# Performance work log

Hardware: AMD Instinct MI355X
Metric: run time of the kernel (lower is better)

Reference implementation:

```python
import jax, jax.numpy as jnp
import numpy as np
from jax import lax

P = (8, 10)        # partition size (p0, p1) for all four types
NUM_HEADS = 32
CURV = 1.0
EPS = 1e-5


def _ln(x, w, b):
    m = x.mean(-1, keepdims=True)
    v = ((x - m) ** 2).mean(-1, keepdims=True)
    return (x - m) / jnp.sqrt(v + EPS) * w + b


def _partition(x, p, mode):
    B, c, T, V = x.shape
    p0, p1 = p
    if mode == 1:
        y = x.reshape(B, c, T // p0, p0, V // p1, p1).transpose(0, 2, 4, 3, 5, 1)
    elif mode == 2:
        y = x.reshape(B, c, T // p0, p0, p1, V // p1).transpose(0, 2, 5, 3, 4, 1)
    elif mode == 3:
        y = x.reshape(B, c, p0, T // p0, V // p1, p1).transpose(0, 3, 4, 2, 5, 1)
    else:
        y = x.reshape(B, c, p0, T // p0, p1, V // p1).transpose(0, 3, 5, 2, 4, 1)
    return y.reshape(-1, p0, p1, c)


def _reverse(parts, B, TV, p, mode):
    T, V = TV
    p0, p1 = p
    y = parts.reshape(B, T // p0, V // p1, p0, p1, -1)
    perm = {1: (0, 5, 1, 3, 2, 4), 2: (0, 5, 1, 3, 4, 2),
            3: (0, 5, 3, 1, 2, 4), 4: (0, 5, 3, 1, 4, 2)}[mode]
    return y.transpose(perm).reshape(B, -1, T, V)


def _euc_to_poincare(x):
    n = jnp.maximum(jnp.linalg.norm(x, axis=-1, keepdims=True), 1e-10)
    return (-1.0 / CURV) * jnp.tanh(-CURV * n) * x / n


def _poincare_to_euc(x):
    n = jnp.clip(jnp.linalg.norm(x, axis=-1, keepdims=True), 1e-10, 1 - 1e-5)
    return jnp.arctanh(n * (-1.0 / CURV)) * x / n


def _linear_attention(x, h):
    # x: [Bw, N, 3*h*d]  (fused qkv channels)
    Bw, N, c3 = x.shape
    d = c3 // (3 * h)
    qkv = x.reshape(Bw, N, 3, h, d).transpose(2, 0, 3, 1, 4)  # [3,Bw,h,N,d]
    q = qkv[0] * (h ** -0.5)
    k, v = qkv[1], qkv[2]
    kv = jax.nn.softmax(jnp.einsum('bhnd,bhne->bhde', k, v), axis=-1)  # [Bw,h,d,d]
    attn = jnp.einsum('bhni,bhmi->bhnm', q, kv)                        # q @ kv^T
    return attn.transpose(0, 2, 1, 3).reshape(Bw, N, h * d)


def setup_inputs() -> dict:
    key = jax.random.key(0)
    ks = jax.random.split(key, 8)
    B, C, T, V = 32, 256, 64, 50
    s = 0.02
    return {
        'x': jax.random.normal(ks[0], (B, C, T, V), jnp.float32),
        'norm1_w': jnp.ones((C,), jnp.float32),
        'norm1_b': jnp.zeros((C,), jnp.float32),
        'map_w': jax.random.normal(ks[1], (C, 2 * C), jnp.float32) * s,
        'map_b': jnp.zeros((2 * C,), jnp.float32),
        'gconv': jax.random.normal(ks[2], (NUM_HEADS // 4, V, V), jnp.float32) * s,
        'tconv_w': jax.random.normal(ks[3], (C // 4, (C // 4) // (NUM_HEADS // 4), 7, 1), jnp.float32) * s,
        'tconv_b': jnp.zeros((C // 4,), jnp.float32),
        'proj_w': jax.random.normal(ks[4], (C, C), jnp.float32) * s,
        'proj_b': jnp.zeros((C,), jnp.float32),
        'norm2_w': jnp.ones((C,), jnp.float32),
        'norm2_b': jnp.zeros((C,), jnp.float32),
        'mlp_w1': jax.random.normal(ks[5], (C, 4 * C), jnp.float32) * s,
        'mlp_b1': jnp.zeros((4 * C,), jnp.float32),
        'mlp_w2': jax.random.normal(ks[6], (4 * C, C), jnp.float32) * s,
        'mlp_b2': jnp.zeros((C,), jnp.float32),
    }


def reference(x, norm1_w, norm1_b, map_w, map_b, gconv, tconv_w, tconv_b,
              proj_w, proj_b, norm2_w, norm2_b, mlp_w1, mlp_b1, mlp_w2, mlp_b2):
    B, C, T, V = x.shape
    xi = x.transpose(0, 2, 3, 1)                 # [B,T,V,C]
    skip = xi
    f = (_ln(xi, norm1_w, norm1_b) @ map_w + map_b).transpose(0, 3, 1, 2)  # [B,2C,T,V]
    f_conv, f_attn = f[:, :C // 2], f[:, C // 2:]
    fg, ft = f_conv[:, :C // 4], f_conv[:, C // 4:]
    G = gconv.shape[0]
    # learned graph conv over joints V (grouped over channels)
    y_g = jnp.einsum('bgctu,gvu->bgctv', fg.reshape(B, G, -1, T, V), gconv).reshape(B, -1, T, V)
    # grouped temporal conv (kernel_size x 1)
    y_t = lax.conv_general_dilated(ft, tconv_w, (1, 1), [(3, 3), (0, 0)],
                                   dimension_numbers=('NCHW', 'OIHW', 'NCHW'),
                                   feature_group_count=G) + tconv_b[None, :, None, None]
    ys = [y_g, y_t]
    ca = f_attn.shape[1] // 4                    # 3C/8 per branch (fused qkv)
    h = NUM_HEADS // 8
    for i in range(4):
        fa = f_attn[:, i * ca:(i + 1) * ca]
        parts = _partition(fa, P, i + 1).reshape(-1, P[0] * P[1], ca)
        a = _poincare_to_euc(_linear_attention(_euc_to_poincare(parts), h))
        ys.append(_reverse(a, B, (T, V), P, i + 1))
    out = jnp.concatenate(ys, axis=1).transpose(0, 2, 3, 1) @ proj_w + proj_b
    out = skip + out
    hmid = jax.nn.gelu(_ln(out, norm2_w, norm2_b) @ mlp_w1 + mlp_b1, approximate=False)
    out = out + (hmid @ mlp_w2 + mlp_b2)
    return out.transpose(0, 3, 1, 2)
```

## Files before the change

### kernel.cpp

```cpp
#include <hip/hip_runtime.h>
#include <hip/hip_bf16.h>
#include <math.h>

#define BB  32
#define TVV 3200
#define XB  819200

typedef __attribute__((ext_vector_type(8))) short s8v;
typedef __attribute__((ext_vector_type(4))) float f4v;
typedef unsigned short u16;
typedef unsigned int   u32;

__device__ __forceinline__ u16 f2bf(float f) {
  __hip_bfloat16 h = __float2bfloat16(f);
  union { __hip_bfloat16 h; u16 u; } cv; cv.h = h; return cv.u;
}
__device__ __forceinline__ float bf2f(u16 u) {
  return __uint_as_float(((u32)u) << 16);
}

__device__ __forceinline__ void glds16(const u16* g, u16* l) {
  __builtin_amdgcn_global_load_lds((const __attribute__((address_space(1))) u32*)g,
                                   (__attribute__((address_space(3))) u32*)l, 16, 0, 0);
}

template<int K>
__device__ __forceinline__ void gemm_core(const u16* __restrict__ A, const u16* __restrict__ B,
                                          int m0, int n0, u16* sA, u16* sB, f4v (&acc)[4][4]) {
  const int tid = threadIdx.x, lane = tid & 63, wave = tid >> 6;
  const int wr = wave >> 1, wc = wave & 1;
  const int q = lane >> 4, l15 = lane & 15;
  const int srow = lane >> 2;
  const int skq  = (lane & 3) << 3;
  const u16* gA = A + (size_t)(m0 + wave * 32 + srow) * K + skq;
  const u16* gB = B + (size_t)(n0 + wave * 32 + srow) * K + skq;
  u16* lA = sA + wave * 1024;
  u16* lB = sB + wave * 1024;
  for (int k0 = 0; k0 < K; k0 += 32) {
    glds16(gA + k0,                 lA);
    glds16(gA + k0 + (size_t)16 * K, lA + 512);
    glds16(gB + k0,                 lB);
    glds16(gB + k0 + (size_t)16 * K, lB + 512);
    __syncthreads();
    s8v af[4], bfr[4];
#pragma unroll
    for (int i = 0; i < 4; ++i) {
      af[i]  = *(const s8v*)(sA + (wr * 64 + i * 16 + l15) * 32 + q * 8);
      bfr[i] = *(const s8v*)(sB + (wc * 64 + i * 16 + l15) * 32 + q * 8);
    }
#pragma unroll
    for (int mi = 0; mi < 4; ++mi)
#pragma unroll
      for (int ni = 0; ni < 4; ++ni)
        acc[mi][ni] = __builtin_amdgcn_mfma_f32_16x16x32_bf16(af[mi], bfr[ni], acc[mi][ni], 0, 0, 0);
    __syncthreads();
  }
}

__global__ __launch_bounds__(256)
void k_wprep(const float* __restrict__ src, u16* __restrict__ dst, int K, int N) {
  int idx = blockIdx.x * 256 + threadIdx.x;
  if (idx >= N * K) return;
  int n = idx / K, k = idx - n * K;
  dst[idx] = f2bf(src[(size_t)k * N + n]);
}

__global__ __launch_bounds__(256)
void k_lnx(const float* __restrict__ x, int b0, const float* __restrict__ w,
           const float* __restrict__ bias, float* __restrict__ xtok, u16* __restrict__ xln) {
  __shared__ float sx[32][264];
  __shared__ float srs_[32][33], srq_[32][33];
  __shared__ float smu[32], sst[32];
  int m0 = blockIdx.x * 32;
  int b = b0 + m0 / TVV, tv0 = m0 % TVV;
  int tid = threadIdx.x;
  int qd = tid & 7, c = tid >> 3;
  const float* xb = x + (size_t)b * XB + tv0;
  float wreg = w[tid], breg = bias[tid];
  float s[4] = {0.f, 0.f, 0.f, 0.f}, ss[4] = {0.f, 0.f, 0.f, 0.f};
#pragma unroll
  for (int k = 0; k < 8; ++k) {
    int cc = k * 32 + c;
    float4 vv = *(const float4*)(xb + (size_t)cc * TVV + qd * 4);
    sx[qd * 4 + 0][cc] = vv.x; sx[qd * 4 + 1][cc] = vv.y;
    sx[qd * 4 + 2][cc] = vv.z; sx[qd * 4 + 3][cc] = vv.w;
    s[0] += vv.x; s[1] += vv.y; s[2] += vv.z; s[3] += vv.w;
    ss[0] += vv.x * vv.x; ss[1] += vv.y * vv.y; ss[2] += vv.z * vv.z; ss[3] += vv.w * vv.w;
  }
#pragma unroll
  for (int i = 0; i < 4; ++i) { srs_[qd * 4 + i][c] = s[i]; srq_[qd * 4 + i][c] = ss[i]; }
  __syncthreads();
  if (tid < 32) {
    float t1 = 0.f, t2 = 0.f;
#pragma unroll
    for (int j = 0; j < 32; ++j) { t1 += srs_[tid][j]; t2 += srq_[tid][j]; }
    float mu = t1 * (1.f / 256.f);
    smu[tid] = mu;
    sst[tid] = rsqrtf(t2 * (1.f / 256.f) - mu * mu + 1e-5f);
  }
  __syncthreads();
  for (int tok = 0; tok < 32; ++tok) {
    float val = sx[tok][tid];
    float mu = smu[tok], rs = sst[tok];
    size_t m = (size_t)(m0 + tok) * 256 + tid;
    xtok[m] = val;
    xln[m]  = f2bf((val - mu) * rs * wreg + breg);
  }
}

__global__ __launch_bounds__(256)
void k_ln(const float* __restrict__ src, const float* __restrict__ w, const float* __restrict__ b,
          u16* __restrict__ dst) {
  int tid = threadIdx.x;
  int tk = tid >> 2, p = tid & 3;
  size_t m = (size_t)blockIdx.x * 64 + tk;
  const float4* row = (const float4*)(src + m * 256 + p * 64);
  float4 r[16];
  float s = 0.f, ss = 0.f;
#pragma unroll
  for (int j = 0; j < 16; ++j) {
    r[j] = row[j];
    s  += r[j].x + r[j].y + r[j].z + r[j].w;
    ss += r[j].x*r[j].x + r[j].y*r[j].y + r[j].z*r[j].z + r[j].w*r[j].w;
  }
  __shared__ float sb1[256], sb2[256];
  sb1[tid] = s; sb2[tid] = ss;
  __syncthreads();
  int base = tk << 2;
  s  = sb1[base] + sb1[base+1] + sb1[base+2] + sb1[base+3];
  ss = sb2[base] + sb2[base+1] + sb2[base+2] + sb2[base+3];
  float mu = s * (1.f / 256.f);
  float rstd = rsqrtf(ss * (1.f / 256.f) - mu * mu + 1e-5f);
  ushort4* drow = (ushort4*)(dst + m * 256 + p * 64);
#pragma unroll
  for (int j = 0; j < 16; ++j) {
    int c = p * 64 + j * 4;
    ushort4 o;
    o.x = f2bf((r[j].x - mu) * rstd * w[c]     + b[c]);
    o.y = f2bf((r[j].y - mu) * rstd * w[c + 1] + b[c + 1]);
    o.z = f2bf((r[j].z - mu) * rstd * w[c + 2] + b[c + 2]);
    o.w = f2bf((r[j].w - mu) * rstd * w[c + 3] + b[c + 3]);
    drow[j] = o;
  }
}

__global__ __launch_bounds__(256)
void k_gemm_map(const u16* __restrict__ xln, const u16* __restrict__ wT,
                const float* __restrict__ bias, u16* __restrict__ f) {
  __shared__ __align__(16) u16 sm[8192];
  int m0 = blockIdx.x * 128, n0 = blockIdx.y * 128;
  f4v acc[4][4];
#pragma unroll
  for (int i = 0; i < 4; ++i)
#pragma unroll
    for (int j = 0; j < 4; ++j) acc[i][j] = (f4v){0.f, 0.f, 0.f, 0.f};
  gemm_core<256>(xln, wT, m0, n0, sm, sm + 4096, acc);
  const int tid = threadIdx.x, lane = tid & 63, wave = tid >> 6;
  const int wr = wave >> 1, wc = wave & 1, q = lane >> 4, l15 = lane & 15;
#pragma unroll
  for (int ni = 0; ni < 4; ++ni) {
    int n = n0 + wc * 64 + ni * 16 + l15;
    float bz = bias[n];
#pragma unroll
    for (int mi = 0; mi < 4; ++mi) {
      int m = m0 + wr * 64 + mi * 16 + q * 4;
#pragma unroll
      for (int rr = 0; rr < 4; ++rr)
        f[(size_t)(m + rr) * 512 + n] = f2bf(acc[mi][ni][rr] + bz);
    }
  }
}

__global__ __launch_bounds__(256)
void k_gemm_proj(const u16* __restrict__ ycat, const u16* __restrict__ wT,
                 const float* __restrict__ bias, float* __restrict__ out1) {
  __shared__ __align__(16) u16 sm[8192];
  int m0 = blockIdx.x * 128, n0 = blockIdx.y * 128;
  f4v acc[4][4];
#pragma unroll
  for (int i = 0; i < 4; ++i)
#pragma unroll
    for (int j = 0; j < 4; ++j) acc[i][j] = (f4v){0.f, 0.f, 0.f, 0.f};
  gemm_core<256>(ycat, wT, m0, n0, sm, sm + 4096, acc);
  const int tid = threadIdx.x, lane = tid & 63, wave = tid >> 6;
  const int wr = wave >> 1, wc = wave & 1, q = lane >> 4, l15 = lane & 15;
#pragma unroll
  for (int ni = 0; ni < 4; ++ni) {
    int n = n0 + wc * 64 + ni * 16 + l15;
    float bz = bias[n];
#pragma unroll
    for (int mi = 0; mi < 4; ++mi) {
      int m = m0 + wr * 64 + mi * 16 + q * 4;
#pragma unroll
      for (int rr = 0; rr < 4; ++rr) {
        size_t idx = (size_t)(m + rr) * 256 + n;
        out1[idx] = out1[idx] + acc[mi][ni][rr] + bz;
      }
    }
  }
}

__global__ __launch_bounds__(256)
void k_gemm_mlp1(const u16* __restrict__ xln2, const u16* __restrict__ wT,
                 const float* __restrict__ bias, u16* __restrict__ hmid) {
  __shared__ __align__(16) u16 sm[8192];
  int m0 = blockIdx.x * 128, n0 = blockIdx.y * 128;
  f4v acc[4][4];
#pragma unroll
  for (int i = 0; i < 4; ++i)
#pragma unroll
    for (int j = 0; j < 4; ++j) acc[i][j] = (f4v){0.f, 0.f, 0.f, 0.f};
  gemm_core<256>(xln2, wT, m0, n0, sm, sm + 4096, acc);
  const int tid = threadIdx.x, lane = tid & 63, wave = tid >> 6;
  const int wr = wave >> 1, wc = wave & 1, q = lane >> 4, l15 = lane & 15;
#pragma unroll
  for (int ni = 0; ni < 4; ++ni) {
    int n = n0 + wc * 64 + ni * 16 + l15;
    float bz = bias[n];
#pragma unroll
    for (int mi = 0; mi < 4; ++mi) {
      int m = m0 + wr * 64 + mi * 16 + q * 4;
#pragma unroll
      for (int rr = 0; rr < 4; ++rr) {
        float h = acc[mi][ni][rr] + bz;
        float g = 0.5f * h * (1.f + erff(h * 0.70710678118654752f));
        hmid[(size_t)(m + rr) * 1024 + n] = f2bf(g);
      }
    }
  }
}

__global__ __launch_bounds__(256)
void k_gemm_mlp2(const u16* __restrict__ hmid, const u16* __restrict__ wT,
                 const float* __restrict__ bias, const float* __restrict__ out1,
                 float* __restrict__ out, int b0) {
  __shared__ __align__(16) u16 sm[10240];
  int m0 = blockIdx.x * 128, n0 = blockIdx.y * 128;
  f4v acc[4][4];
#pragma unroll
  for (int i = 0; i < 4; ++i)
#pragma unroll
    for (int j = 0; j < 4; ++j) acc[i][j] = (f4v){0.f, 0.f, 0.f, 0.f};
  gemm_core<1024>(hmid, wT, m0, n0, sm, sm + 4096, acc);
  const int tid = threadIdx.x, lane = tid & 63, wave = tid >> 6;
  const int wr = wave >> 1, wc = wave & 1, q = lane >> 4, l15 = lane & 15;
  float* twv = (float*)sm + wave * 16 * 65;
  int mbase = m0 + wr * 64;
  int bglob = b0 + mbase / TVV;
  int tvb = mbase % TVV;
  for (int ni = 0; ni < 4; ++ni) {
    int n = n0 + wc * 64 + ni * 16 + l15;
    float bz = bias[n];
#pragma unroll
    for (int mi = 0; mi < 4; ++mi) {
      int ml = mi * 16 + q * 4;
#pragma unroll
      for (int rr = 0; rr < 4; ++rr) {
        int m = mbase + ml + rr;
        twv[l15 * 65 + ml + rr] = acc[mi][ni][rr] + bz + out1[(size_t)m * 256 + n];
      }
    }
    __syncthreads();
#pragma unroll
    for (int np = 0; np < 16; ++np) {
      int n2 = n0 + wc * 64 + ni * 16 + np;
      out[((size_t)bglob * 256 + n2) * TVV + tvb + lane] = twv[np * 65 + lane];
    }
    __syncthreads();
  }
}

__global__ __launch_bounds__(256)
void k_gconv(const u16* __restrict__ f, const float* __restrict__ gw,
             u16* __restrict__ ycat) {
  __shared__ float sf[50][64];
  int bc = blockIdx.x >> 6, t = blockIdx.x & 63;
  int tid = threadIdx.x;
  size_t tok0 = (size_t)bc * TVV + t * 50;
  for (int idx = tid; idx < 3200; idx += 256) {
    int u = idx >> 6, oc = idx & 63;
    sf[u][oc] = bf2f(f[(tok0 + u) * 512 + oc]);
  }
  __syncthreads();
  for (int idx = tid; idx < 3200; idx += 256) {
    int v = idx >> 6, oc = idx & 63;
    const float* gr = gw + ((size_t)(oc >> 3) * 50 + v) * 50;
    float s = 0.f;
#pragma unroll 10
    for (int u = 0; u < 50; ++u) s += sf[u][oc] * gr[u];
    ycat[(tok0 + v) * 256 + oc] = f2bf(s);
  }
}

__global__ __launch_bounds__(256)
void k_tconv(const u16* __restrict__ f, const float* __restrict__ tw,
             const float* __restrict__ tb, u16* __restrict__ ycat) {
  __shared__ float sw[64 * 57];
  int bc = blockIdx.x >> 6, t = blockIdx.x & 63;
  int tid = threadIdx.x;
  for (int idx = tid; idx < 64 * 56; idx += 256) {
    int oc = idx / 56, k = idx - oc * 56;
    sw[oc * 57 + k] = tw[idx];
  }
  __syncthreads();
  size_t base = (size_t)bc * TVV;
  for (int idx = tid; idx < 3200; idx += 256) {
    int v = idx >> 6, oc = idx & 63;
    int g = oc >> 3;
    float s = tb[oc];
#pragma unroll
    for (int kt = 0; kt < 7; ++kt) {
      int ts = t + kt - 3;
      if (ts < 0 || ts >= 64) continue;
      s8v fv = *(const s8v*)(f + (base + ts * 50 + v) * 512 + 64 + g * 8);
      const float* wr_ = sw + oc * 57 + kt;
#pragma unroll
      for (int ic = 0; ic < 8; ++ic) s += bf2f((u16)fv[ic]) * wr_[ic * 7];
    }
    ycat[(base + t * 50 + v) * 256 + 64 + oc] = f2bf(s);
  }
}

__global__ __launch_bounds__(256)
void k_attn(const u16* __restrict__ f, u16* __restrict__ ycat) {
  int mode = blockIdx.z, bc = blockIdx.y;
  int wt = blockIdx.x / 5, wv = blockIdx.x % 5;
  __shared__ float parts[80][97];
  __shared__ float kvb[256];
  __shared__ float obuf[80][33];
  __shared__ float scl[80];
  int tid = threadIdx.x;
  size_t base = (size_t)bc * TVV;
  int ch0 = 128 + mode * 96;
  for (int idx = tid; idx < 80 * 96; idx += 256) {
    int n = idx / 96, ch = idx - n * 96;
    int lt = n / 10, lv = n - lt * 10;
    int t = (mode < 2) ? (wt * 8 + lt) : (lt * 8 + wt);
    int v = ((mode & 1) == 0) ? (wv * 10 + lv) : (lv * 5 + wv);
    parts[n][ch] = bf2f(f[(base + t * 50 + v) * 512 + ch0 + ch]);
  }
  __syncthreads();
  if (tid < 80) {
    float s = 0.f;
    for (int ch = 0; ch < 96; ++ch) { float val = parts[tid][ch]; s += val * val; }
    float nrm = fmaxf(sqrtf(s), 1e-10f);
    float sc = tanhf(nrm) / nrm;
    for (int ch = 0; ch < 96; ++ch) parts[tid][ch] *= sc;
  }
  __syncthreads();
  {
    int h = tid >> 6, dd = (tid >> 3) & 7, e = tid & 7;
    float s = 0.f;
    for (int n = 0; n < 80; ++n)
      s += parts[n][32 + h * 8 + dd] * parts[n][64 + h * 8 + e];
    kvb[tid] = s;
  }
  __syncthreads();
  if (tid < 32) {
    int h = tid >> 3, dd = tid & 7;
    float* r = &kvb[h * 64 + dd * 8];
    float mx = r[0];
    for (int e = 1; e < 8; ++e) mx = fmaxf(mx, r[e]);
    float ex[8]; float sm2 = 0.f;
    for (int e = 0; e < 8; ++e) { ex[e] = expf(r[e] - mx); sm2 += ex[e]; }
    float inv = 1.f / sm2;
    for (int e = 0; e < 8; ++e) r[e] = ex[e] * inv;
  }
  __syncthreads();
  for (int idx = tid; idx < 80 * 32; idx += 256) {
    int n = idx >> 5, cc = idx & 31;
    int h = cc >> 3, m_ = cc & 7;
    float s = 0.f;
#pragma unroll
    for (int i = 0; i < 8; ++i)
      s += parts[n][h * 8 + i] * kvb[h * 64 + m_ * 8 + i];
    obuf[n][cc] = s * 0.5f;
  }
  __syncthreads();
  if (tid < 80) {
    float s = 0.f;
    for (int cc = 0; cc < 32; ++cc) { float val = obuf[tid][cc]; s += val * val; }
    float nn = sqrtf(s);
    nn = fminf(fmaxf(nn, 1e-10f), 1.f - 1e-5f);
    scl[tid] = -atanhf(nn) / nn;
  }
  __syncthreads();
  for (int idx = tid; idx < 80 * 32; idx += 256) {
    int n = idx >> 5, cc = idx & 31;
    int lt = n / 10, lv = n - lt * 10;
    int t = (mode < 2) ? (wt * 8 + lt) : (lt * 8 + wt);
    int v = ((mode & 1) == 0) ? (wv * 10 + lv) : (lv * 5 + wv);
    ycat[(base + t * 50 + v) * 256 + 128 + mode * 32 + cc] = f2bf(obuf[n][cc] * scl[n]);
  }
}

extern "C" void kernel_launch(void* const* d_in, const int* in_sizes, int n_in,
                              void* d_out, int out_size, void* d_ws, size_t ws_size,
                              hipStream_t stream) {
  const float* x       = (const float*)d_in[0];
  const float* n1w     = (const float*)d_in[1];
  const float* n1b     = (const float*)d_in[2];
  const float* map_w   = (const float*)d_in[3];
  const float* map_b   = (const float*)d_in[4];
  const float* gconv   = (const float*)d_in[5];
  const float* tconv_w = (const float*)d_in[6];
  const float* tconv_b = (const float*)d_in[7];
  const float* proj_w  = (const float*)d_in[8];
  const float* proj_b  = (const float*)d_in[9];
  const float* n2w     = (const float*)d_in[10];
  const float* n2b     = (const float*)d_in[11];
  const float* w1      = (const float*)d_in[12];
  const float* b1      = (const float*)d_in[13];
  const float* w2      = (const float*)d_in[14];
  const float* b2      = (const float*)d_in[15];
  float* out = (float*)d_out;

  const size_t WB = (size_t)(512 * 256 + 256 * 256 + 1024 * 256 + 256 * 1024) * 2;
  int CH = 32;
  while (CH > 1 && (size_t)CH * TVV * 4096 + WB > ws_size) CH >>= 1;
  if ((size_t)CH * TVV * 4096 + WB > ws_size) return;
  const int Mc = CH * TVV;
  const int nch = BB / CH;

  char* ws = (char*)d_ws;
  float* xtok   = (float*)ws;
  u16* f        = (u16*)(ws + (size_t)Mc * 1024);
  u16* hmid     = f;
  u16* xln      = (u16*)(ws + (size_t)Mc * 3072);
  u16* ycat     = (u16*)(ws + (size_t)Mc * 3584);
  u16* wmapT    = (u16*)(ws + (size_t)Mc * 4096);
  u16* wprojT   = wmapT + 512 * 256;
  u16* w1T      = wprojT + 256 * 256;
  u16* w2T      = w1T + 1024 * 256;

  k_wprep<<<dim3(512), 256, 0, stream>>>(map_w, wmapT, 256, 512);
  k_wprep<<<dim3(256), 256, 0, stream>>>(proj_w, wprojT, 256, 256);
  k_wprep<<<dim3(1024), 256, 0, stream>>>(w1, w1T, 256, 1024);
  k_wprep<<<dim3(1024), 256, 0, stream>>>(w2, w2T, 1024, 256);

  for (int c = 0; c < nch; ++c) {
    int b0 = c * CH;
    k_lnx<<<dim3(Mc / 32), 256, 0, stream>>>(x, b0, n1w, n1b, xtok, xln);
    k_gemm_map<<<dim3(Mc / 128, 4), 256, 0, stream>>>(xln, wmapT, map_b, f);
    k_gconv<<<dim3(CH * 64), 256, 0, stream>>>(f, gconv, ycat);
    k_tconv<<<dim3(CH * 64), 256, 0, stream>>>(f, tconv_w, tconv_b, ycat);
    k_attn<<<dim3(40, CH, 4), 256, 0, stream>>>(f, ycat);
    k_gemm_proj<<<dim3(Mc / 128, 2), 256, 0, stream>>>(ycat, wprojT, proj_b, xtok);
    k_ln<<<dim3(Mc / 64), 256, 0, stream>>>(xtok, n2w, n2b, xln);
    k_gemm_mlp1<<<dim3(Mc / 128, 8), 256, 0, stream>>>(xln, w1T, b1, hmid);
    k_gemm_mlp2<<<dim3(Mc / 128, 2), 256, 0, stream>>>(hmid, w2T, b2, xtok, out, b0);
  }
}
```

Before: 1.010 ms.

## Swizzle GEMM LDS layout and parallelize attention row-norm reductions

```diff
diff --git a/kernel.cpp b/kernel.cpp
--- a/kernel.cpp
+++ b/kernel.cpp
@@ -31,22 +31,23 @@
   const int wr = wave >> 1, wc = wave & 1;
   const int q = lane >> 4, l15 = lane & 15;
   const int srow = lane >> 2;
-  const int skq  = (lane & 3) << 3;
-  const u16* gA = A + (size_t)(m0 + wave * 32 + srow) * K + skq;
-  const u16* gB = B + (size_t)(n0 + wave * 32 + srow) * K + skq;
+  const int sslot = (lane & 3) ^ ((lane >> 3) & 3);
+  const u16* gA = A + (size_t)(m0 + wave * 32 + srow) * K + sslot * 8;
+  const u16* gB = B + (size_t)(n0 + wave * 32 + srow) * K + sslot * 8;
   u16* lA = sA + wave * 1024;
   u16* lB = sB + wave * 1024;
+  const int sw = ((l15 >> 1) & 3) << 3;
   for (int k0 = 0; k0 < K; k0 += 32) {
-    glds16(gA + k0,                 lA);
+    glds16(gA + k0,                  lA);
     glds16(gA + k0 + (size_t)16 * K, lA + 512);
-    glds16(gB + k0,                 lB);
+    glds16(gB + k0,                  lB);
     glds16(gB + k0 + (size_t)16 * K, lB + 512);
     __syncthreads();
     s8v af[4], bfr[4];
 #pragma unroll
     for (int i = 0; i < 4; ++i) {
-      af[i]  = *(const s8v*)(sA + (wr * 64 + i * 16 + l15) * 32 + q * 8);
-      bfr[i] = *(const s8v*)(sB + (wc * 64 + i * 16 + l15) * 32 + q * 8);
+      af[i]  = *(const s8v*)(sA + (wr * 64 + i * 16 + l15) * 32 + ((q << 3) ^ sw));
+      bfr[i] = *(const s8v*)(sB + (wc * 64 + i * 16 + l15) * 32 + ((q << 3) ^ sw));
     }
 #pragma unroll
     for (int mi = 0; mi < 4; ++mi)
@@ -329,6 +330,7 @@
   __shared__ float kvb[256];
   __shared__ float obuf[80][33];
   __shared__ float scl[80];
+  __shared__ float pp[80][4];
   int tid = threadIdx.x;
   size_t base = (size_t)bc * TVV;
   int ch0 = 128 + mode * 96;
@@ -340,12 +342,24 @@
     parts[n][ch] = bf2f(f[(base + t * 50 + v) * 512 + ch0 + ch]);
   }
   __syncthreads();
+  for (int idx = tid; idx < 320; idx += 256) {
+    int n = idx >> 2, p = idx & 3;
+    const float* pr = &parts[n][p * 24];
+    float s = 0.f;
+#pragma unroll
+    for (int ch = 0; ch < 24; ++ch) { float val = pr[ch]; s += val * val; }
+    pp[n][p] = s;
+  }
+  __syncthreads();
   if (tid < 80) {
-    float s = 0.f;
-    for (int ch = 0; ch < 96; ++ch) { float val = parts[tid][ch]; s += val * val; }
+    float s = pp[tid][0] + pp[tid][1] + pp[tid][2] + pp[tid][3];
     float nrm = fmaxf(sqrtf(s), 1e-10f);
-    float sc = tanhf(nrm) / nrm;
-    for (int ch = 0; ch < 96; ++ch) parts[tid][ch] *= sc;
+    scl[tid] = tanhf(nrm) / nrm;
+  }
+  __syncthreads();
+  for (int idx = tid; idx < 80 * 96; idx += 256) {
+    int n = idx / 96, ch = idx - n * 96;
+    parts[n][ch] *= scl[n];
   }
   __syncthreads();
   {
@@ -377,10 +391,17 @@
     obuf[n][cc] = s * 0.5f;
   }
   __syncthreads();
+  for (int idx = tid; idx < 160; idx += 256) {
+    int n = idx >> 1, p = idx & 1;
+    const float* orow = &obuf[n][p * 16];
+    float s = 0.f;
+#pragma unroll
+    for (int cc = 0; cc < 16; ++cc) { float val = orow[cc]; s += val * val; }
+    pp[n][p] = s;
+  }
+  __syncthreads();
   if (tid < 80) {
-    float s = 0.f;
-    for (int cc = 0; cc < 32; ++cc) { float val = obuf[tid][cc]; s += val * val; }
-    float nn = sqrtf(s);
+    float nn = sqrtf(pp[tid][0] + pp[tid][1]);
     nn = fminf(fmaxf(nn, 1e-10f), 1.f - 1e-5f);
     scl[tid] = -atanhf(nn) / nn;
   }
```

After: 1.009 ms. Within noise of the previous version (-0.1%).
